# Optimization experiments

Measured on AMD Instinct MI355X. Metric: run time of the kernel, lower is better.

## Reference

```python
import jax, jax.numpy as jnp
import numpy as np

NUM_NEIGH = 6  # 5 + 1 hardcoded in PeerNet

def pr_transform(h, num_neigh=NUM_NEIGH):
    # h: [B, F]. For each feature column, replace each value by the mean of its
    # num_neigh nearest batch values (by absolute difference, self included).
    def per_feat(col):  # col: [B]
        dist = jnp.abs(col[:, None] - col[None, :])  # [B, B]
        _, idx = jax.lax.top_k(-dist, num_neigh)      # [B, k] nearest indices
        return jnp.mean(col[idx], axis=1)             # [B]
    # lax.map over features keeps peak memory at one [B,B] matrix at a time
    return jax.lax.map(per_feat, h.T).T


def setup_inputs() -> dict:
    key = jax.random.key(0)
    ks = jax.random.split(key, 9)
    B, D = 4096, 1024
    H1, H2, O = 128, 64, 2
    s = 0.02
    return {
        "x":   jax.random.normal(ks[0], (B, D), dtype=jnp.float32),
        "W1":  jax.random.normal(ks[1], (H1, D), dtype=jnp.float32) * s,
        "b1":  jnp.zeros((H1,), dtype=jnp.float32),
        "Wpr": jax.random.normal(ks[2], (H1, H1), dtype=jnp.float32) * s,
        "bpr": jnp.zeros((H1,), dtype=jnp.float32),
        "W2":  jax.random.normal(ks[3], (H2, H1), dtype=jnp.float32) * s,
        "b2":  jnp.zeros((H2,), dtype=jnp.float32),
        "Wo":  jax.random.normal(ks[4], (O, H2), dtype=jnp.float32) * s,
        "bo":  jnp.zeros((O,), dtype=jnp.float32),
    }


def reference(x, W1, b1, Wpr, bpr, W2, b2, Wo, bo):
    # hidden1 + relu (dropout = identity, eval mode)
    h1 = jax.nn.relu(x @ W1.T + b1)               # [B, 128]
    # PRLayer: per-feature kNN averaging over batch, then linear
    pr = pr_transform(h1)                          # [B, 128]
    pr = jax.nn.relu(pr @ Wpr.T + bpr)             # [B, 128]
    h2 = jax.nn.relu(pr @ W2.T + b2)               # [B, 64]
    out = h2 @ Wo.T + bo                           # [B, 2]
    return out
```

## Files before the change

### kernel.cpp

```cpp
#include <hip/hip_runtime.h>


#define NB   4096
#define DIN  1024
#define NH1  128
#define NH2  64

#define PAD(p) ((p) + ((p) >> 3))

typedef _Float16 f16x8 __attribute__((ext_vector_type(8)));
typedef _Float16 f16x4 __attribute__((ext_vector_type(4)));
typedef float    f32x4 __attribute__((ext_vector_type(4)));

__device__ __forceinline__ unsigned pack_hl(float x) {
    const _Float16 h = (_Float16)x;
    const _Float16 l = (_Float16)(x - (float)h);
    unsigned short hu, lu;
    __builtin_memcpy(&hu, &h, 2);
    __builtin_memcpy(&lu, &l, 2);
    return (unsigned)hu | ((unsigned)lu << 16);
}

__device__ __forceinline__ void unpack8(const unsigned* __restrict__ p,
                                        f16x8& hv, f16x8& lv) {
#pragma unroll
    for (int q = 0; q < 8; ++q) {
        const unsigned u = p[q];
        const unsigned short hu = (unsigned short)(u & 0xffffu);
        const unsigned short lu = (unsigned short)(u >> 16);
        _Float16 h, l;
        __builtin_memcpy(&h, &hu, 2);
        __builtin_memcpy(&l, &lu, 2);
        hv[q] = h; lv[q] = l;
    }
}

__global__ __launch_bounds__(512) void gemm1_mfma(const float* __restrict__ x,
                                                  const float* __restrict__ W1,
                                                  const float* __restrict__ b1,
                                                  float* __restrict__ h1T)
{
    __shared__ _Float16 xhi[16 * 1032];
    __shared__ _Float16 xlo[16 * 1032];
    const int tid = threadIdx.x;
    const int m0  = blockIdx.x * 16;

    {
        const int r  = tid >> 5;
        const int kb = (tid & 31) * 4;
#pragma unroll
        for (int i = 0; i < 8; ++i) {
            const int k = kb + i * 128;
            const float4 v = *(const float4*)&x[(size_t)(m0 + r) * DIN + k];
            const _Float16 h0 = (_Float16)v.x, h1 = (_Float16)v.y;
            const _Float16 h2 = (_Float16)v.z, h3 = (_Float16)v.w;
            f16x4 hv = {h0, h1, h2, h3};
            f16x4 lv = {(_Float16)(v.x - (float)h0), (_Float16)(v.y - (float)h1),
                        (_Float16)(v.z - (float)h2), (_Float16)(v.w - (float)h3)};
            *(f16x4*)&xhi[r * 1032 + k] = hv;
            *(f16x4*)&xlo[r * 1032 + k] = lv;
        }
    }
    __syncthreads();

    const int lane = tid & 63;
    const int w    = tid >> 6;
    const int n0   = w * 16;
    const int fr   = lane & 15;
    const int fq   = lane >> 4;

    f32x4 acc = {0.f, 0.f, 0.f, 0.f};
    const float* __restrict__ wp = &W1[(size_t)(n0 + fr) * DIN + fq * 8];
    const _Float16* xh = &xhi[fr * 1032 + fq * 8];
    const _Float16* xl = &xlo[fr * 1032 + fq * 8];

#pragma unroll 4
    for (int ks = 0; ks < 32; ++ks) {
        const int k = ks * 32;
        const f16x8 ah = *(const f16x8*)&xh[k];
        const f16x8 al = *(const f16x8*)&xl[k];
        const float4 wa = *(const float4*)&wp[k];
        const float4 wb = *(const float4*)&wp[k + 4];
        const float wf[8] = {wa.x, wa.y, wa.z, wa.w, wb.x, wb.y, wb.z, wb.w};
        f16x8 bh, bl;
#pragma unroll
        for (int q = 0; q < 8; ++q) {
            const _Float16 h = (_Float16)wf[q];
            bh[q] = h;
            bl[q] = (_Float16)(wf[q] - (float)h);
        }
        acc = __builtin_amdgcn_mfma_f32_16x16x32_f16(ah, bh, acc, 0, 0, 0);
        acc = __builtin_amdgcn_mfma_f32_16x16x32_f16(ah, bl, acc, 0, 0, 0);
        acc = __builtin_amdgcn_mfma_f32_16x16x32_f16(al, bh, acc, 0, 0, 0);
    }

    const int n = n0 + fr;
    const float bv = b1[n];
    float4 o;
    o.x = fmaxf(acc[0] + bv, 0.f);
    o.y = fmaxf(acc[1] + bv, 0.f);
    o.z = fmaxf(acc[2] + bv, 0.f);
    o.w = fmaxf(acc[3] + bv, 0.f);
    *(float4*)&h1T[(size_t)n * NB + m0 + fq * 4] = o;
}

__global__ __launch_bounds__(512) void sort_window_kernel(const float* __restrict__ h1T,
                                                          float* __restrict__ prtT)
{
    __shared__ float s[PAD(NB - 1) + 2];
    __shared__ float r_[PAD(NB - 1) + 2];
    const int t    = threadIdx.x;
    const int col  = blockIdx.x >> 1;
    const int half = blockIdx.x & 1;
    const float* __restrict__ src = h1T + (size_t)col * NB;

    float v[8];
    {
        const float4 a = *(const float4*)&src[8 * t];
        const float4 b = *(const float4*)&src[8 * t + 4];
        v[0] = a.x; v[1] = a.y; v[2] = a.z; v[3] = a.w;
        v[4] = b.x; v[5] = b.y; v[6] = b.z; v[7] = b.w;
    }

#define CE(a, b, up)                                        \
    {                                                       \
        const float _x = v[a], _y = v[b];                   \
        v[a] = (up) ? fminf(_x, _y) : fmaxf(_x, _y);        \
        v[b] = (up) ? fmaxf(_x, _y) : fminf(_x, _y);        \
    }

    CE(0, 1, true); CE(2, 3, false); CE(4, 5, true); CE(6, 7, false);
    CE(0, 2, true);  CE(1, 3, true);  CE(4, 6, false); CE(5, 7, false);
    CE(0, 1, true);  CE(2, 3, true);  CE(4, 5, false); CE(6, 7, false);

#pragma unroll
    for (int k = 8; k <= 256; k <<= 1) {
        const bool up = (t & (k >> 3)) == 0;
#pragma unroll
        for (int j = k >> 1; j >= 8; j >>= 1) {
            const int  m       = j >> 3;
            const bool keepmin = (((t & m) == 0) == up);
#pragma unroll
            for (int q = 0; q < 8; ++q) {
                const float p = __shfl_xor(v[q], m);
                v[q] = keepmin ? fminf(v[q], p) : fmaxf(v[q], p);
            }
        }
        CE(0, 4, up); CE(1, 5, up); CE(2, 6, up); CE(3, 7, up);
        CE(0, 2, up); CE(1, 3, up); CE(4, 6, up); CE(5, 7, up);
        CE(0, 1, up); CE(2, 3, up); CE(4, 5, up); CE(6, 7, up);
    }

#pragma unroll
    for (int k = 512; k <= 4096; k <<= 1) {
        const bool up = (t & (k >> 3)) == 0;
#pragma unroll
        for (int j = k >> 1; j >= 512; j >>= 1) {
            __syncthreads();
            float4 w0 = {v[0], v[1], v[2], v[3]};
            float4 w1 = {v[4], v[5], v[6], v[7]};
            *(float4*)&s[9 * t]     = w0;
            *(float4*)&s[9 * t + 4] = w1;
            __syncthreads();
            const int tp = t ^ (j >> 3);
            const float4 pa = *(const float4*)&s[9 * tp];
            const float4 pb = *(const float4*)&s[9 * tp + 4];
            const bool keepmin = (((t & (j >> 3)) == 0) == up);
            const float p[8] = {pa.x, pa.y, pa.z, pa.w, pb.x, pb.y, pb.z, pb.w};
#pragma unroll
            for (int q = 0; q < 8; ++q)
                v[q] = keepmin ? fminf(v[q], p[q]) : fmaxf(v[q], p[q]);
        }
#pragma unroll
        for (int j = 256; j >= 8; j >>= 1) {
            const int  m       = j >> 3;
            const bool keepmin = (((t & m) == 0) == up);
#pragma unroll
            for (int q = 0; q < 8; ++q) {
                const float p = __shfl_xor(v[q], m);
                v[q] = keepmin ? fminf(v[q], p) : fmaxf(v[q], p);
            }
        }
        CE(0, 4, up); CE(1, 5, up); CE(2, 6, up); CE(3, 7, up);
        CE(0, 2, up); CE(1, 3, up); CE(4, 6, up); CE(5, 7, up);
        CE(0, 1, up); CE(2, 3, up); CE(4, 5, up); CE(6, 7, up);
    }
#undef CE

    __syncthreads();
    {
        float4 w0 = {v[0], v[1], v[2], v[3]};
        float4 w1 = {v[4], v[5], v[6], v[7]};
        *(float4*)&s[9 * t]     = w0;
        *(float4*)&s[9 * t + 4] = w1;
    }
    __syncthreads();

    if (v[7] == 0.0f) {
        const float4 z4 = {0.f, 0.f, 0.f, 0.f};
        *(float4*)&r_[9 * t]     = z4;
        *(float4*)&r_[9 * t + 4] = z4;
    } else {
        float rr[8];
#pragma unroll
        for (int q = 0; q < 8; ++q) {
            const int  p  = 8 * t + q;
            const float v0 = v[q];
            int l = p, h = p;
            float sum = v0;
#pragma unroll
            for (int it = 0; it < 5; ++it) {
                const int li = (l > 0) ? l - 1 : 0;
                const int ri = (h < NB - 1) ? h + 1 : NB - 1;
                const float sl = s[PAD(li)];
                const float sr = s[PAD(ri)];
                const float dl = (l > 0) ? (v0 - sl) : 1e30f;
                const float dr = (h < NB - 1) ? (sr - v0) : 1e30f;
                if (dl <= dr) { sum += sl; l = li; }
                else          { sum += sr; h = ri; }
            }
            rr[q] = sum * (1.0f / 6.0f);
        }
        const float4 r0 = {rr[0], rr[1], rr[2], rr[3]};
        const float4 r1 = {rr[4], rr[5], rr[6], rr[7]};
        *(float4*)&r_[9 * t]     = r0;
        *(float4*)&r_[9 * t + 4] = r1;
    }
    __syncthreads();

    const float z5 = s[PAD(5)];
    float v0[4];
    bool  zs[4];
    float key[4];
    int   lo[4], hi[4];
#pragma unroll
    for (int w = 0; w < 4; ++w) {
        const int e = half * 2048 + t + w * 512;
        v0[w]  = src[e];
        zs[w]  = (v0[w] == 0.0f) && (z5 == 0.0f);
        key[w] = zs[w] ? -1.0f : v0[w];
        lo[w]  = 0;
        hi[w]  = NB;
    }
#pragma unroll
    for (int step = 0; step < 12; ++step) {
#pragma unroll
        for (int w = 0; w < 4; ++w) {
            const int mid = (lo[w] + hi[w]) >> 1;
            const float sv = s[PAD(mid)];
            if (sv < key[w]) lo[w] = mid + 1; else hi[w] = mid;
        }
    }
#pragma unroll
    for (int w = 0; w < 4; ++w) {
        const int e = half * 2048 + t + w * 512;
        const float res = zs[w] ? 0.0f : r_[PAD(lo[w])];
        prtT[(size_t)col * NB + e] = res;
    }
}

__global__ __launch_bounds__(512) void tail_kernel(const float* __restrict__ AT,
                                                   const float* __restrict__ Wpr,
                                                   const float* __restrict__ bpr,
                                                   const float* __restrict__ W2,
                                                   const float* __restrict__ b2,
                                                   const float* __restrict__ Wo,
                                                   const float* __restrict__ bo,
                                                   float* __restrict__ out)
{
    __shared__ unsigned Apk[16 * 132];
    __shared__ unsigned Ppk[16 * 132];
    __shared__ float    Rs[64 * 32];
    const int tid = threadIdx.x;
    const int m0  = blockIdx.x * 16;

    {
        const int k = tid >> 2;
        const int f = (tid & 3) * 4;
        const float4 v = *(const float4*)&AT[(size_t)k * NB + m0 + f];
        const float vf[4] = {v.x, v.y, v.z, v.w};
#pragma unroll
        for (int j = 0; j < 4; ++j)
            Apk[(f + j) * 132 + k] = pack_hl(vf[j]);
    }
    __syncthreads();

    const int lane = tid & 63;
    const int w    = tid >> 6;
    const int fr   = lane & 15;
    const int fq   = lane >> 4;

    {
        const int n0 = w * 16;
        f32x4 acc = {0.f, 0.f, 0.f, 0.f};
        const float*    __restrict__ wp = &Wpr[(size_t)(n0 + fr) * NH1 + fq * 8];
        const unsigned* __restrict__ ap = &Apk[fr * 132 + fq * 8];
#pragma unroll
        for (int ks = 0; ks < 4; ++ks) {
            const int k = ks * 32;
            f16x8 ah, al;
            unpack8(&ap[k], ah, al);
            const float4 wa = *(const float4*)&wp[k];
            const float4 wb = *(const float4*)&wp[k + 4];
            const float wf[8] = {wa.x, wa.y, wa.z, wa.w, wb.x, wb.y, wb.z, wb.w};
            f16x8 bh, bl;
#pragma unroll
            for (int q = 0; q < 8; ++q) {
                const _Float16 h = (_Float16)wf[q];
                bh[q] = h;
                bl[q] = (_Float16)(wf[q] - (float)h);
            }
            acc = __builtin_amdgcn_mfma_f32_16x16x32_f16(ah, bh, acc, 0, 0, 0);
            acc = __builtin_amdgcn_mfma_f32_16x16x32_f16(ah, bl, acc, 0, 0, 0);
            acc = __builtin_amdgcn_mfma_f32_16x16x32_f16(al, bh, acc, 0, 0, 0);
        }
        const int n = n0 + fr;
        const float bv = bpr[n];
#pragma unroll
        for (int j = 0; j < 4; ++j) {
            const float p = fmaxf(acc[j] + bv, 0.f);
            Ppk[(fq * 4 + j) * 132 + n] = pack_hl(p);
        }
    }
    __syncthreads();

    if (w < 4) {
        const int j0 = w * 16;
        f32x4 acc2 = {0.f, 0.f, 0.f, 0.f};
        const float*    __restrict__ w2p = &W2[(size_t)(j0 + fr) * NH1 + fq * 8];
        const unsigned* __restrict__ pp  = &Ppk[fr * 132 + fq * 8];
#pragma unroll
        for (int ks = 0; ks < 4; ++ks) {
            const int k = ks * 32;
            f16x8 ah, al;
            unpack8(&pp[k], ah, al);
            const float4 wa = *(const float4*)&w2p[k];
            const float4 wb = *(const float4*)&w2p[k + 4];
            const float wf[8] = {wa.x, wa.y, wa.z, wa.w, wb.x, wb.y, wb.z, wb.w};
            f16x8 bh, bl;
#pragma unroll
            for (int q = 0; q < 8; ++q) {
                const _Float16 h = (_Float16)wf[q];
                bh[q] = h;
                bl[q] = (_Float16)(wf[q] - (float)h);
            }
            acc2 = __builtin_amdgcn_mfma_f32_16x16x32_f16(ah, bh, acc2, 0, 0, 0);
            acc2 = __builtin_amdgcn_mfma_f32_16x16x32_f16(ah, bl, acc2, 0, 0, 0);
            acc2 = __builtin_amdgcn_mfma_f32_16x16x32_f16(al, bh, acc2, 0, 0, 0);
        }
        const int jj  = j0 + fr;
        const float b2v = b2[jj];
        const float wo0 = Wo[jj];
        const float wo1 = Wo[NH2 + jj];
        const int g = w * 16 + fr;
#pragma unroll
        for (int j = 0; j < 4; ++j) {
            const float h = fmaxf(acc2[j] + b2v, 0.f);
            const int m = fq * 4 + j;
            Rs[g * 32 + m * 2 + 0] = h * wo0;
            Rs[g * 32 + m * 2 + 1] = h * wo1;
        }
    }
    __syncthreads();

    if (tid < 32) {
        const int mm = tid >> 1, o = tid & 1;
        float sum = 0.f;
#pragma unroll
        for (int g = 0; g < 64; ++g) sum += Rs[g * 32 + mm * 2 + o];
        out[(size_t)(m0 + mm) * 2 + o] = sum + bo[o];
    }
}

extern "C" void kernel_launch(void* const* d_in, const int* in_sizes, int n_in,
                              void* d_out, int out_size, void* d_ws, size_t ws_size,
                              hipStream_t stream)
{
    const float* x   = (const float*)d_in[0];
    const float* W1  = (const float*)d_in[1];
    const float* b1  = (const float*)d_in[2];
    const float* Wpr = (const float*)d_in[3];
    const float* bpr = (const float*)d_in[4];
    const float* W2  = (const float*)d_in[5];
    const float* b2  = (const float*)d_in[6];
    const float* Wo  = (const float*)d_in[7];
    const float* bo  = (const float*)d_in[8];

    float* ws     = (float*)d_ws;
    float* h1T    = ws;
    float* prtT   = h1T + NH1 * NB;

    gemm1_mfma<<<dim3(NB / 16), 512, 0, stream>>>(x, W1, b1, h1T);
    sort_window_kernel<<<dim3(NH1 * 2), 512, 0, stream>>>(h1T, prtT);
    tail_kernel<<<dim3(NB / 16), 512, 0, stream>>>(prtT, Wpr, bpr, W2, b2, Wo, bo,
                                                   (float*)d_out);
}
```

Baseline: 47.27 us.

## Sort 16 elements per thread with 256-thread blocks in sort kernel

The bitonic sort in the per-feature window kernel now gives each thread 16 register elements instead of 8, launched with 256 threads per block. More of the sort runs as in-register compare-exchanges and fewer stages need shuffles or LDS round trips with block barriers. The shared-memory padding changes to match the 17-float stride. The cost is more registers per thread and half as many threads per block for the window and binary-search phases, which may reduce latency hiding.

```diff
diff --git a/kernel.cpp b/kernel.cpp
--- a/kernel.cpp
+++ b/kernel.cpp
@@ -6,7 +6,7 @@
 #define NH1  128
 #define NH2  64
 
-#define PAD(p) ((p) + ((p) >> 3))
+#define PAD16(p) ((p) + ((p) >> 4))
 
 typedef _Float16 f16x8 __attribute__((ext_vector_type(8)));
 typedef _Float16 f16x4 __attribute__((ext_vector_type(4)));
@@ -104,22 +104,22 @@
     *(float4*)&h1T[(size_t)n * NB + m0 + fq * 4] = o;
 }
 
-__global__ __launch_bounds__(512) void sort_window_kernel(const float* __restrict__ h1T,
+__global__ __launch_bounds__(256) void sort_window_kernel(const float* __restrict__ h1T,
                                                           float* __restrict__ prtT)
 {
-    __shared__ float s[PAD(NB - 1) + 2];
-    __shared__ float r_[PAD(NB - 1) + 2];
+    __shared__ float s[PAD16(NB - 1) + 2];
+    __shared__ float r_[PAD16(NB - 1) + 2];
     const int t    = threadIdx.x;
     const int col  = blockIdx.x >> 1;
     const int half = blockIdx.x & 1;
     const float* __restrict__ src = h1T + (size_t)col * NB;
 
-    float v[8];
-    {
-        const float4 a = *(const float4*)&src[8 * t];
-        const float4 b = *(const float4*)&src[8 * t + 4];
-        v[0] = a.x; v[1] = a.y; v[2] = a.z; v[3] = a.w;
-        v[4] = b.x; v[5] = b.y; v[6] = b.z; v[7] = b.w;
+    float v[16];
+#pragma unroll
+    for (int i4 = 0; i4 < 4; ++i4) {
+        const float4 a = *(const float4*)&src[16 * t + i4 * 4];
+        v[i4 * 4 + 0] = a.x; v[i4 * 4 + 1] = a.y;
+        v[i4 * 4 + 2] = a.z; v[i4 * 4 + 3] = a.w;
     }
 
 #define CE(a, b, up)                                        \
@@ -128,83 +128,93 @@
         v[a] = (up) ? fminf(_x, _y) : fmaxf(_x, _y);        \
         v[b] = (up) ? fmaxf(_x, _y) : fminf(_x, _y);        \
     }
-
-    CE(0, 1, true); CE(2, 3, false); CE(4, 5, true); CE(6, 7, false);
-    CE(0, 2, true);  CE(1, 3, true);  CE(4, 6, false); CE(5, 7, false);
-    CE(0, 1, true);  CE(2, 3, true);  CE(4, 5, false); CE(6, 7, false);
-
-#pragma unroll
-    for (int k = 8; k <= 256; k <<= 1) {
-        const bool up = (t & (k >> 3)) == 0;
-#pragma unroll
-        for (int j = k >> 1; j >= 8; j >>= 1) {
-            const int  m       = j >> 3;
+#define INTRA8(up)                                                          \
+    CE(0, 8, up); CE(1, 9, up); CE(2, 10, up); CE(3, 11, up);               \
+    CE(4, 12, up); CE(5, 13, up); CE(6, 14, up); CE(7, 15, up);             \
+    CE(0, 4, up); CE(1, 5, up); CE(2, 6, up); CE(3, 7, up);                 \
+    CE(8, 12, up); CE(9, 13, up); CE(10, 14, up); CE(11, 15, up);           \
+    CE(0, 2, up); CE(1, 3, up); CE(4, 6, up); CE(5, 7, up);                 \
+    CE(8, 10, up); CE(9, 11, up); CE(12, 14, up); CE(13, 15, up);           \
+    CE(0, 1, up); CE(2, 3, up); CE(4, 5, up); CE(6, 7, up);                 \
+    CE(8, 9, up); CE(10, 11, up); CE(12, 13, up); CE(14, 15, up);
+
+    CE(0, 1, true);  CE(2, 3, false); CE(4, 5, true);   CE(6, 7, false);
+    CE(8, 9, true);  CE(10, 11, false); CE(12, 13, true); CE(14, 15, false);
+    CE(0, 2, true);  CE(1, 3, true);  CE(4, 6, false);  CE(5, 7, false);
+    CE(8, 10, true); CE(9, 11, true); CE(12, 14, false); CE(13, 15, false);
+    CE(0, 1, true);  CE(2, 3, true);  CE(4, 5, false);  CE(6, 7, false);
+    CE(8, 9, true);  CE(10, 11, true); CE(12, 13, false); CE(14, 15, false);
+    CE(0, 4, true);  CE(1, 5, true);  CE(2, 6, true);   CE(3, 7, true);
+    CE(8, 12, false); CE(9, 13, false); CE(10, 14, false); CE(11, 15, false);
+    CE(0, 2, true);  CE(1, 3, true);  CE(4, 6, true);   CE(5, 7, true);
+    CE(8, 10, false); CE(9, 11, false); CE(12, 14, false); CE(13, 15, false);
+    CE(0, 1, true);  CE(2, 3, true);  CE(4, 5, true);   CE(6, 7, true);
+    CE(8, 9, false); CE(10, 11, false); CE(12, 13, false); CE(14, 15, false);
+    {
+        const bool up = (t & 1) == 0;
+        INTRA8(up)
+    }
+
+#pragma unroll
+    for (int k = 32; k <= 4096; k <<= 1) {
+        const bool up = (t & (k >> 4)) == 0;
+#pragma unroll
+        for (int j = k >> 1; j >= 1024; j >>= 1) {
+            __syncthreads();
+#pragma unroll
+            for (int i4 = 0; i4 < 4; ++i4) {
+                float4 wv = {v[i4 * 4 + 0], v[i4 * 4 + 1],
+                             v[i4 * 4 + 2], v[i4 * 4 + 3]};
+                *(float4*)&s[17 * t + i4 * 4] = wv;
+            }
+            __syncthreads();
+            const int tp = t ^ (j >> 4);
+            const bool keepmin = (((t & (j >> 4)) == 0) == up);
+            float p[16];
+#pragma unroll
+            for (int i4 = 0; i4 < 4; ++i4) {
+                const float4 pa = *(const float4*)&s[17 * tp + i4 * 4];
+                p[i4 * 4 + 0] = pa.x; p[i4 * 4 + 1] = pa.y;
+                p[i4 * 4 + 2] = pa.z; p[i4 * 4 + 3] = pa.w;
+            }
+#pragma unroll
+            for (int q = 0; q < 16; ++q)
+                v[q] = keepmin ? fminf(v[q], p[q]) : fmaxf(v[q], p[q]);
+        }
+#pragma unroll
+        for (int j = ((k >> 1) > 512 ? 512 : (k >> 1)); j >= 16; j >>= 1) {
+            const int  m       = j >> 4;
             const bool keepmin = (((t & m) == 0) == up);
 #pragma unroll
-            for (int q = 0; q < 8; ++q) {
+            for (int q = 0; q < 16; ++q) {
                 const float p = __shfl_xor(v[q], m);
                 v[q] = keepmin ? fminf(v[q], p) : fmaxf(v[q], p);
             }
         }
-        CE(0, 4, up); CE(1, 5, up); CE(2, 6, up); CE(3, 7, up);
-        CE(0, 2, up); CE(1, 3, up); CE(4, 6, up); CE(5, 7, up);
-        CE(0, 1, up); CE(2, 3, up); CE(4, 5, up); CE(6, 7, up);
-    }
-
-#pragma unroll
-    for (int k = 512; k <= 4096; k <<= 1) {
-        const bool up = (t & (k >> 3)) == 0;
-#pragma unroll
-        for (int j = k >> 1; j >= 512; j >>= 1) {
-            __syncthreads();
-            float4 w0 = {v[0], v[1], v[2], v[3]};
-            float4 w1 = {v[4], v[5], v[6], v[7]};
-            *(float4*)&s[9 * t]     = w0;
-            *(float4*)&s[9 * t + 4] = w1;
-            __syncthreads();
-            const int tp = t ^ (j >> 3);
-            const float4 pa = *(const float4*)&s[9 * tp];
-            const float4 pb = *(const float4*)&s[9 * tp + 4];
-            const bool keepmin = (((t & (j >> 3)) == 0) == up);
-            const float p[8] = {pa.x, pa.y, pa.z, pa.w, pb.x, pb.y, pb.z, pb.w};
-#pragma unroll
-            for (int q = 0; q < 8; ++q)
-                v[q] = keepmin ? fminf(v[q], p[q]) : fmaxf(v[q], p[q]);
-        }
-#pragma unroll
-        for (int j = 256; j >= 8; j >>= 1) {
-            const int  m       = j >> 3;
-            const bool keepmin = (((t & m) == 0) == up);
-#pragma unroll
-            for (int q = 0; q < 8; ++q) {
-                const float p = __shfl_xor(v[q], m);
-                v[q] = keepmin ? fminf(v[q], p) : fmaxf(v[q], p);
-            }
-        }
-        CE(0, 4, up); CE(1, 5, up); CE(2, 6, up); CE(3, 7, up);
-        CE(0, 2, up); CE(1, 3, up); CE(4, 6, up); CE(5, 7, up);
-        CE(0, 1, up); CE(2, 3, up); CE(4, 5, up); CE(6, 7, up);
-    }
+        INTRA8(up)
+    }
+#undef INTRA8
 #undef CE
 
     __syncthreads();
-    {
-        float4 w0 = {v[0], v[1], v[2], v[3]};
-        float4 w1 = {v[4], v[5], v[6], v[7]};
-        *(float4*)&s[9 * t]     = w0;
-        *(float4*)&s[9 * t + 4] = w1;
-    }
-    __syncthreads();
-
-    if (v[7] == 0.0f) {
+#pragma unroll
+    for (int i4 = 0; i4 < 4; ++i4) {
+        float4 wv = {v[i4 * 4 + 0], v[i4 * 4 + 1],
+                     v[i4 * 4 + 2], v[i4 * 4 + 3]};
+        *(float4*)&s[17 * t + i4 * 4] = wv;
+    }
+    __syncthreads();
+
+    if (v[15] == 0.0f) {
         const float4 z4 = {0.f, 0.f, 0.f, 0.f};
-        *(float4*)&r_[9 * t]     = z4;
-        *(float4*)&r_[9 * t + 4] = z4;
+#pragma unroll
+        for (int i4 = 0; i4 < 4; ++i4)
+            *(float4*)&r_[17 * t + i4 * 4] = z4;
     } else {
-        float rr[8];
-#pragma unroll
-        for (int q = 0; q < 8; ++q) {
-            const int  p  = 8 * t + q;
+        float rr[16];
+#pragma unroll
+        for (int q = 0; q < 16; ++q) {
+            const int  p  = 16 * t + q;
             const float v0 = v[q];
             int l = p, h = p;
             float sum = v0;
@@ -212,8 +222,8 @@
             for (int it = 0; it < 5; ++it) {
                 const int li = (l > 0) ? l - 1 : 0;
                 const int ri = (h < NB - 1) ? h + 1 : NB - 1;
-                const float sl = s[PAD(li)];
-                const float sr = s[PAD(ri)];
+                const float sl = s[PAD16(li)];
+                const float sr = s[PAD16(ri)];
                 const float dl = (l > 0) ? (v0 - sl) : 1e30f;
                 const float dr = (h < NB - 1) ? (sr - v0) : 1e30f;
                 if (dl <= dr) { sum += sl; l = li; }
@@ -221,21 +231,23 @@
             }
             rr[q] = sum * (1.0f / 6.0f);
         }
-        const float4 r0 = {rr[0], rr[1], rr[2], rr[3]};
-        const float4 r1 = {rr[4], rr[5], rr[6], rr[7]};
-        *(float4*)&r_[9 * t]     = r0;
-        *(float4*)&r_[9 * t + 4] = r1;
-    }
-    __syncthreads();
-
-    const float z5 = s[PAD(5)];
-    float v0[4];
-    bool  zs[4];
-    float key[4];
-    int   lo[4], hi[4];
-#pragma unroll
-    for (int w = 0; w < 4; ++w) {
-        const int e = half * 2048 + t + w * 512;
+#pragma unroll
+        for (int i4 = 0; i4 < 4; ++i4) {
+            float4 rv = {rr[i4 * 4 + 0], rr[i4 * 4 + 1],
+                         rr[i4 * 4 + 2], rr[i4 * 4 + 3]};
+            *(float4*)&r_[17 * t + i4 * 4] = rv;
+        }
+    }
+    __syncthreads();
+
+    const float z5 = s[PAD16(5)];
+    float v0[8];
+    bool  zs[8];
+    float key[8];
+    int   lo[8], hi[8];
+#pragma unroll
+    for (int w = 0; w < 8; ++w) {
+        const int e = half * 2048 + t + w * 256;
         v0[w]  = src[e];
         zs[w]  = (v0[w] == 0.0f) && (z5 == 0.0f);
         key[w] = zs[w] ? -1.0f : v0[w];
@@ -245,16 +257,16 @@
 #pragma unroll
     for (int step = 0; step < 12; ++step) {
 #pragma unroll
-        for (int w = 0; w < 4; ++w) {
+        for (int w = 0; w < 8; ++w) {
             const int mid = (lo[w] + hi[w]) >> 1;
-            const float sv = s[PAD(mid)];
+            const float sv = s[PAD16(mid)];
             if (sv < key[w]) lo[w] = mid + 1; else hi[w] = mid;
         }
     }
 #pragma unroll
-    for (int w = 0; w < 4; ++w) {
-        const int e = half * 2048 + t + w * 512;
-        const float res = zs[w] ? 0.0f : r_[PAD(lo[w])];
+    for (int w = 0; w < 8; ++w) {
+        const int e = half * 2048 + t + w * 256;
+        const float res = zs[w] ? 0.0f : r_[PAD16(lo[w])];
         prtT[(size_t)col * NB + e] = res;
     }
 }
@@ -391,7 +403,7 @@
     float* prtT   = h1T + NH1 * NB;
 
     gemm1_mfma<<<dim3(NB / 16), 512, 0, stream>>>(x, W1, b1, h1T);
-    sort_window_kernel<<<dim3(NH1 * 2), 512, 0, stream>>>(h1T, prtT);
+    sort_window_kernel<<<dim3(NH1 * 2), 256, 0, stream>>>(h1T, prtT);
     tail_kernel<<<dim3(NB / 16), 512, 0, stream>>>(prtT, Wpr, bpr, W2, b2, Wo, bo,
                                                    (float*)d_out);
 }
```

After: 51.59 us. +9.1%, slower.
